# Kernel tuning notes

Measured on AMD Instinct MI355X. Metric: run time of the kernel, lower is better.

The kernel has to match this reference:

```python
import jax, jax.numpy as jnp
import numpy as np

TOP_K = 2


def setup_inputs() -> dict:
    key = jax.random.key(0)
    k1, k2, k3, k4, k5 = jax.random.split(key, 5)
    B, S, D, E, F = 2, 1024, 2048, 8, 768
    scale_in = 1.0 / np.sqrt(D)
    scale_ff = 1.0 / np.sqrt(F)
    return {
        "x": jax.random.normal(k1, (B, S, D), dtype=jnp.float32),
        "w_gate_router": jax.random.normal(k2, (E, D), dtype=jnp.float32) * scale_in,
        "w_gate_proj": jax.random.normal(k3, (E, F, D), dtype=jnp.float32) * scale_in,
        "w_up_proj": jax.random.normal(k4, (E, F, D), dtype=jnp.float32) * scale_in,
        "w_down_proj": jax.random.normal(k5, (E, D, F), dtype=jnp.float32) * scale_ff,
    }


def moe_forward(x, w_gate_router, w_gate_proj, w_up_proj, w_down_proj):
    E = w_gate_router.shape[0]
    # Router: scores [B,S,E], top-k selection, softmax over the k selected scores.
    scores = jnp.einsum("bsd,ed->bse", x, w_gate_router)
    topk_scores, topk_idx = jax.lax.top_k(scores, TOP_K)          # [B,S,K]
    topk_probs = jax.nn.softmax(topk_scores, axis=-1)             # [B,S,K]
    # Dense combine weights: zero for unselected experts (== scatter of topk_probs).
    weights = jnp.sum(topk_probs[..., None] * jax.nn.one_hot(topk_idx, E, dtype=x.dtype), axis=-2)  # [B,S,E]
    # Per-expert SwiGLU computed densely over all tokens (same math as
    # gather/dispatch-per-expert followed by scatter-add combine).
    gate = jnp.einsum("bsd,efd->bsef", x, w_gate_proj)            # [B,S,E,F]
    up = jnp.einsum("bsd,efd->bsef", x, w_up_proj)
    hidden = jax.nn.silu(gate) * up                                # [B,S,E,F]
    # Weighted combine: sum_e weights[b,s,e] * (hidden @ w_down[e].T)
    out = jnp.einsum("bsef,edf,bse->bsd", hidden, w_down_proj, weights)
    return out


def reference(x, w_gate_router, w_gate_proj, w_up_proj, w_down_proj):
    return moe_forward(x, w_gate_router, w_gate_proj, w_up_proj, w_down_proj)
```

## Files before the change

kernel.cpp:

```cpp
#include <hip/hip_runtime.h>

#define T_TOK 2048
#define DIM   2048
#define NEXP  8
#define FF    768
#define NGRP  16
#define BK    64

typedef unsigned short u16;
typedef unsigned int   u32;
typedef __bf16 bf16x8 __attribute__((ext_vector_type(8)));
typedef float  f32x4  __attribute__((ext_vector_type(4)));
typedef u16    u16x4  __attribute__((ext_vector_type(4)));
typedef u16    u16x8  __attribute__((ext_vector_type(8)));

#define AS1 __attribute__((address_space(1)))
#define AS3 __attribute__((address_space(3)))

__device__ __forceinline__ u16 f2bf(float f) {
    union { u32 i; float f; } v; v.f = f;
    u32 r = v.i + 0x7FFF + ((v.i >> 16) & 1);
    return (u16)(r >> 16);
}
__device__ __forceinline__ float bf2f(u16 u) {
    union { u32 i; float f; } v; v.i = ((u32)u) << 16; return v.f;
}

__device__ __forceinline__ void gload16(const u16* g, u16* l) {
    __builtin_amdgcn_global_load_lds((const AS1 u32*)g, (AS3 u32*)l, 16, 0, 0);
}

__global__ void cvt3_kernel(const float* __restrict__ s0, u16* __restrict__ d0,
                            const float* __restrict__ s1, u16* __restrict__ d1,
                            const float* __restrict__ s2, u16* __restrict__ d2, int n4) {
    const float* s; u16* d;
    switch (blockIdx.y) {
        case 0: s = s0; d = d0; break;
        case 1: s = s1; d = d1; break;
        default: s = s2; d = d2; break;
    }
    int i = blockIdx.x * blockDim.x + threadIdx.x;
    int st = gridDim.x * blockDim.x;
    for (; i < n4; i += st) {
        f32x4 v = ((const f32x4*)s)[i];
        u16x4 o;
#pragma unroll
        for (int j = 0; j < 4; j++) o[j] = f2bf(v[j]);
        ((u16x4*)d)[i] = o;
    }
}

__global__ void router_kernel(const float* __restrict__ x, const float* __restrict__ wr,
                              int* cnt, int* rt_e, float* rt_p, u16* __restrict__ xb) {
    int wave = threadIdx.x >> 6, lane = threadIdx.x & 63;
    int t = blockIdx.x * 4 + wave;
    float xv[32];
#pragma unroll
    for (int i = 0; i < 32; i++) xv[i] = x[(size_t)t * DIM + i * 64 + lane];
#pragma unroll
    for (int i = 0; i < 32; i++) xb[(size_t)t * DIM + i * 64 + lane] = f2bf(xv[i]);
    float s[NEXP];
#pragma unroll
    for (int e = 0; e < NEXP; e++) {
        float acc = 0.f;
#pragma unroll
        for (int i = 0; i < 32; i++) acc += xv[i] * wr[(size_t)e * DIM + i * 64 + lane];
        for (int off = 32; off; off >>= 1) acc += __shfl_xor(acc, off);
        s[e] = acc;
    }
    if (lane == 0) {
        int bi = 0; float bv = s[0];
        for (int e = 1; e < NEXP; e++) if (s[e] > bv) { bv = s[e]; bi = e; }
        float sv = -1e30f; int si = 0;
        for (int e = 0; e < NEXP; e++) { if (e == bi) continue; if (s[e] > sv) { sv = s[e]; si = e; } }
        float p0 = 1.f / (1.f + __expf(sv - bv));
        float p1 = 1.f - p0;
        rt_e[t * 2 + 0] = bi; rt_e[t * 2 + 1] = si;
        rt_p[t * 2 + 0] = p0; rt_p[t * 2 + 1] = p1;
        atomicAdd(&cnt[bi * 2 + 0], 1);
        atomicAdd(&cnt[si * 2 + 1], 1);
    }
}

__global__ void scan_kernel(const int* cnt, int* base, int* tile_g, int* tile_m0, int* ntiles) {
    int lane = threadIdx.x;
    int c = (lane < NGRP) ? cnt[lane] : 0;
    int nt_g = (c + 127) >> 7;
    int pre = 0, tpre = 0;
    for (int i = 0; i < NGRP; i++) {
        int ci = __shfl(c, i), ti = __shfl(nt_g, i);
        if (i < lane) { pre += ci; tpre += ti; }
    }
    if (lane < NGRP) {
        base[lane] = pre;
        for (int j = 0; j < nt_g; j++) { tile_g[tpre + j] = lane; tile_m0[tpre + j] = j * 128; }
        if (lane == NGRP - 1) *ntiles = tpre + nt_g;
    }
}

__global__ void assign_kernel(const int* rt_e, const float* rt_p, const int* base,
                              int* poscnt, int* rowtok, float* rowprob) {
    int t = blockIdx.x * blockDim.x + threadIdx.x;
    if (t >= T_TOK) return;
    for (int k = 0; k < 2; k++) {
        int g = rt_e[t * 2 + k] * 2 + k;
        int pos = atomicAdd(&poscnt[g], 1);
        int row = base[g] + pos;
        rowtok[row] = t;
        rowprob[row] = rt_p[t * 2 + k];
    }
}

__launch_bounds__(256)
__global__ void gateup_kernel(const u16* __restrict__ xb, const u16* __restrict__ wgb,
                              const u16* __restrict__ wub,
                              const int* cnt, const int* base, const int* tile_g,
                              const int* tile_m0, const int* ntiles,
                              const int* rowtok, const float* rowprob,
                              u16* __restrict__ hidden) {
    int tile = blockIdx.x;
    if (tile >= *ntiles) return;
    int g = tile_g[tile], m0 = tile_m0[tile];
    int e = g >> 1;
    int f0 = blockIdx.y * 32;
    int cg = cnt[g], bg_ = base[g];

    __shared__ u16 As[2][128 * BK];
    __shared__ u16 Bs[2][64 * BK];
    __shared__ int   tks[128];
    __shared__ float ps[128];

    int tid = threadIdx.x;
    if (tid < 128) {
        int valid = (m0 + tid) < cg;
        tks[tid] = valid ? rowtok[bg_ + m0 + tid] : 0;
        ps[tid]  = valid ? rowprob[bg_ + m0 + tid] : 0.f;
    }
    __syncthreads();

    int wave = tid >> 6, lane = tid & 63;
    int quad = lane >> 4, l16 = lane & 15;
    int wr = wave >> 1, wc = wave & 1;

    int r8  = lane >> 3;
    int csw = ((lane & 7) ^ r8) * 8;

    const u16* gA[4]; int lA[4];
#pragma unroll
    for (int gi = 0; gi < 4; gi++) {
        int row = wave * 32 + gi * 8 + r8;
        gA[gi] = xb + (size_t)tks[row] * DIM + csw;
        lA[gi] = (wave * 32 + gi * 8) * BK;
    }
    const u16* bsrc = (wave & 1) ? wub : wgb;
    const u16* gB[2]; int lB[2];
#pragma unroll
    for (int gi = 0; gi < 2; gi++) {
        int f = f0 + (wave >> 1) * 16 + gi * 8 + r8;
        gB[gi] = bsrc + ((size_t)e * FF + f) * DIM + csw;
        lB[gi] = (wave * 16 + gi * 8) * BK;
    }

    f32x4 acc[4][2] = {};

#pragma unroll
    for (int gi = 0; gi < 4; gi++) gload16(gA[gi], &As[0][0] + lA[gi]);
#pragma unroll
    for (int gi = 0; gi < 2; gi++) gload16(gB[gi], &Bs[0][0] + lB[gi]);
    __syncthreads();

    int sw0 = ((0 * 4 + quad) ^ (l16 & 7)) * 8;
    int sw1 = ((1 * 4 + quad) ^ (l16 & 7)) * 8;

#pragma unroll 2
    for (int kt = 0; kt < DIM / BK; kt++) {
        int cur = kt & 1;
        int kk = (kt + 1) * BK;
        if (kk < DIM) {
#pragma unroll
            for (int gi = 0; gi < 4; gi++) gload16(gA[gi] + kk, &As[cur ^ 1][0] + lA[gi]);
#pragma unroll
            for (int gi = 0; gi < 2; gi++) gload16(gB[gi] + kk, &Bs[cur ^ 1][0] + lB[gi]);
        }
#pragma unroll
        for (int ks = 0; ks < 2; ks++) {
            int sw = ks ? sw1 : sw0;
            bf16x8 a[4], b[2];
#pragma unroll
            for (int mi = 0; mi < 4; mi++)
                a[mi] = *(const bf16x8*)&As[cur][(wr * 64 + mi * 16 + l16) * BK + sw];
#pragma unroll
            for (int ni = 0; ni < 2; ni++)
                b[ni] = *(const bf16x8*)&Bs[cur][(wc * 32 + ni * 16 + l16) * BK + sw];
#pragma unroll
            for (int mi = 0; mi < 4; mi++)
#pragma unroll
                for (int ni = 0; ni < 2; ni++)
                    acc[mi][ni] = __builtin_amdgcn_mfma_f32_16x16x32_bf16(a[mi], b[ni], acc[mi][ni], 0, 0, 0);
        }
        __syncthreads();
    }

    int f = f0 + wc * 16 + l16;
#pragma unroll
    for (int mi = 0; mi < 4; mi++) {
#pragma unroll
        for (int r = 0; r < 4; r++) {
            int m = wr * 64 + mi * 16 + quad * 4 + r;
            if (m0 + m < cg) {
                float gv = acc[mi][0][r], uv = acc[mi][1][r];
                float h = (gv / (1.f + __expf(-gv))) * uv * ps[m];
                hidden[(size_t)(bg_ + m0 + m) * FF + f] = f2bf(h);
            }
        }
    }
}

__launch_bounds__(256)
__global__ void down_kernel(const u16* __restrict__ hid, const u16* __restrict__ wdb,
                            const int* cnt, const int* base, const int* tile_g,
                            const int* tile_m0, const int* ntiles, const int* rowtok,
                            u16* __restrict__ out0, u16* __restrict__ out1) {
    int tile = blockIdx.x;
    if (tile >= *ntiles) return;
    int g = tile_g[tile], m0 = tile_m0[tile];
    int e = g >> 1, slot = g & 1;
    int d0 = blockIdx.y * 64;
    int cg = cnt[g], bg_ = base[g];

    __shared__ u16 As[2][128 * BK];
    __shared__ u16 Bs[2][64 * BK];
    __shared__ int tks[128];

    int tid = threadIdx.x;
    if (tid < 128) tks[tid] = ((m0 + tid) < cg) ? rowtok[bg_ + m0 + tid] : 0;
    __syncthreads();

    int wave = tid >> 6, lane = tid & 63;
    int quad = lane >> 4, l16 = lane & 15;
    int wr = wave >> 1, wc = wave & 1;

    int r8  = lane >> 3;
    int csw = ((lane & 7) ^ r8) * 8;

    const u16* gA[4]; int lA[4];
#pragma unroll
    for (int gi = 0; gi < 4; gi++) {
        int row = wave * 32 + gi * 8 + r8;
        gA[gi] = hid + (size_t)(bg_ + m0 + row) * FF + csw;
        lA[gi] = (wave * 32 + gi * 8) * BK;
    }
    const u16* gB[2]; int lB[2];
#pragma unroll
    for (int gi = 0; gi < 2; gi++) {
        int n = wave * 16 + gi * 8 + r8;
        gB[gi] = wdb + ((size_t)e * DIM + d0 + n) * FF + csw;
        lB[gi] = (wave * 16 + gi * 8) * BK;
    }

    f32x4 acc[4][2] = {};

#pragma unroll
    for (int gi = 0; gi < 4; gi++) gload16(gA[gi], &As[0][0] + lA[gi]);
#pragma unroll
    for (int gi = 0; gi < 2; gi++) gload16(gB[gi], &Bs[0][0] + lB[gi]);
    __syncthreads();

    int sw0 = ((0 * 4 + quad) ^ (l16 & 7)) * 8;
    int sw1 = ((1 * 4 + quad) ^ (l16 & 7)) * 8;

#pragma unroll 2
    for (int kt = 0; kt < FF / BK; kt++) {
        int cur = kt & 1;
        int kk = (kt + 1) * BK;
        if (kk < FF) {
#pragma unroll
            for (int gi = 0; gi < 4; gi++) gload16(gA[gi] + kk, &As[cur ^ 1][0] + lA[gi]);
#pragma unroll
            for (int gi = 0; gi < 2; gi++) gload16(gB[gi] + kk, &Bs[cur ^ 1][0] + lB[gi]);
        }
#pragma unroll
        for (int ks = 0; ks < 2; ks++) {
            int sw = ks ? sw1 : sw0;
            bf16x8 a[4], b[2];
#pragma unroll
            for (int mi = 0; mi < 4; mi++)
                a[mi] = *(const bf16x8*)&As[cur][(wr * 64 + mi * 16 + l16) * BK + sw];
#pragma unroll
            for (int ni = 0; ni < 2; ni++)
                b[ni] = *(const bf16x8*)&Bs[cur][(wc * 32 + ni * 16 + l16) * BK + sw];
#pragma unroll
            for (int mi = 0; mi < 4; mi++)
#pragma unroll
                for (int ni = 0; ni < 2; ni++)
                    acc[mi][ni] = __builtin_amdgcn_mfma_f32_16x16x32_bf16(a[mi], b[ni], acc[mi][ni], 0, 0, 0);
        }
        __syncthreads();
    }

    u16* outp = slot ? out1 : out0;
#pragma unroll
    for (int mi = 0; mi < 4; mi++) {
#pragma unroll
        for (int ni = 0; ni < 2; ni++) {
            int d = d0 + wc * 32 + ni * 16 + l16;
#pragma unroll
            for (int r = 0; r < 4; r++) {
                int m = wr * 64 + mi * 16 + quad * 4 + r;
                if (m0 + m < cg) {
                    outp[(size_t)tks[m] * DIM + d] = f2bf(acc[mi][ni][r]);
                }
            }
        }
    }
}

__global__ void combine_kernel(const u16* __restrict__ o0, const u16* __restrict__ o1,
                               float* __restrict__ out) {
    int i = blockIdx.x * blockDim.x + threadIdx.x;
    u16x8 a = *(const u16x8*)(o0 + (size_t)i * 8);
    u16x8 b = *(const u16x8*)(o1 + (size_t)i * 8);
    f32x4 r0, r1;
#pragma unroll
    for (int j = 0; j < 4; j++) {
        r0[j] = bf2f(a[j]) + bf2f(b[j]);
        r1[j] = bf2f(a[4 + j]) + bf2f(b[4 + j]);
    }
    *(f32x4*)(out + (size_t)i * 8) = r0;
    *(f32x4*)(out + (size_t)i * 8 + 4) = r1;
}

extern "C" void kernel_launch(void* const* d_in, const int* in_sizes, int n_in,
                              void* d_out, int out_size, void* d_ws, size_t ws_size,
                              hipStream_t stream) {
    const float* x  = (const float*)d_in[0];
    const float* wr = (const float*)d_in[1];
    const float* wg = (const float*)d_in[2];
    const float* wu = (const float*)d_in[3];
    const float* wd = (const float*)d_in[4];
    float* out = (float*)d_out;

    char* W = (char*)d_ws;
    int*   cnt     = (int*)(W + 0);
    int*   poscnt  = (int*)(W + 64);
    int*   base    = (int*)(W + 128);
    int*   ntiles  = (int*)(W + 192);
    int*   tile_g  = (int*)(W + 256);
    int*   tile_m0 = (int*)(W + 512);
    int*   rt_e    = (int*)(W + 1024);
    float* rt_p    = (float*)(W + 20480);
    int*   rowtok  = (int*)(W + 40960);
    float* rowprob = (float*)(W + 61440);
    u16*   hidden  = (u16*)(W + 81920);
    u16*   xb      = (u16*)(W + ((size_t)8  << 20));
    u16*   wgb     = (u16*)(W + ((size_t)17 << 20));
    u16*   wub     = (u16*)(W + ((size_t)43 << 20));
    u16*   wdb     = (u16*)(W + ((size_t)69 << 20));
    u16*   out0    = (u16*)(W + ((size_t)17 << 20));
    u16*   out1    = (u16*)(W + ((size_t)26 << 20));

    hipMemsetAsync(W, 0, 256, stream);

    const int NW = NEXP * FF * DIM / 4;
    cvt3_kernel<<<dim3(1536, 3), 256, 0, stream>>>(wg, wgb, wu, wub, wd, wdb, NW);

    router_kernel<<<T_TOK / 4, 256, 0, stream>>>(x, wr, cnt, rt_e, rt_p, xb);
    scan_kernel<<<1, 64, 0, stream>>>(cnt, base, tile_g, tile_m0, ntiles);
    assign_kernel<<<8, 256, 0, stream>>>(rt_e, rt_p, base, poscnt, rowtok, rowprob);

    gateup_kernel<<<dim3(48, 24), 256, 0, stream>>>(xb, wgb, wub, cnt, base, tile_g, tile_m0,
                                                    ntiles, rowtok, rowprob, hidden);
    down_kernel<<<dim3(48, 32), 256, 0, stream>>>(hidden, wdb, cnt, base, tile_g, tile_m0,
                                                  ntiles, rowtok, out0, out1);
    combine_kernel<<<T_TOK * DIM / (256 * 8), 256, 0, stream>>>(out0, out1, out);
}
```

Baseline: 369.7 us.

## Fuse router with weight conversion, merge scan/assign, widen GEMM N tiles to 128

The router now runs as an extra grid row of the weight-conversion kernel, and the scan and assign steps share one kernel that uses shared-memory atomics. Together this removes two launches. The gate/up and down GEMM kernels double their N tile (64 gate+up columns, 128 output columns) with a 4x4 MFMA accumulator per wave. This raises reuse of the gathered A tile and halves the grid. The cost is more registers and LDS per block and fewer blocks, which may reduce occupancy and load balance.

Result: no change. 362.5 us (-1.9%).

```diff
diff --git a/kernel.cpp b/kernel.cpp
--- a/kernel.cpp
+++ b/kernel.cpp
@@ -30,14 +30,48 @@
     __builtin_amdgcn_global_load_lds((const AS1 u32*)g, (AS3 u32*)l, 16, 0, 0);
 }
 
-__global__ void cvt3_kernel(const float* __restrict__ s0, u16* __restrict__ d0,
-                            const float* __restrict__ s1, u16* __restrict__ d1,
-                            const float* __restrict__ s2, u16* __restrict__ d2, int n4) {
+__global__ void cvtrouter_kernel(const float* __restrict__ x, const float* __restrict__ wr,
+                                 int* cnt, int* rt_e, float* rt_p, u16* __restrict__ xb,
+                                 const float* __restrict__ wg, u16* __restrict__ wgb,
+                                 const float* __restrict__ wu, u16* __restrict__ wub,
+                                 const float* __restrict__ wd, u16* __restrict__ wdb, int n4) {
+    if (blockIdx.y == 0) {
+        if (blockIdx.x >= T_TOK / 4) return;
+        int wave = threadIdx.x >> 6, lane = threadIdx.x & 63;
+        int t = blockIdx.x * 4 + wave;
+        float xv[32];
+#pragma unroll
+        for (int i = 0; i < 32; i++) xv[i] = x[(size_t)t * DIM + i * 64 + lane];
+#pragma unroll
+        for (int i = 0; i < 32; i++) xb[(size_t)t * DIM + i * 64 + lane] = f2bf(xv[i]);
+        float s[NEXP];
+#pragma unroll
+        for (int e = 0; e < NEXP; e++) {
+            float acc = 0.f;
+#pragma unroll
+            for (int i = 0; i < 32; i++) acc += xv[i] * wr[(size_t)e * DIM + i * 64 + lane];
+            for (int off = 32; off; off >>= 1) acc += __shfl_xor(acc, off);
+            s[e] = acc;
+        }
+        if (lane == 0) {
+            int bi = 0; float bv = s[0];
+            for (int e = 1; e < NEXP; e++) if (s[e] > bv) { bv = s[e]; bi = e; }
+            float sv = -1e30f; int si = 0;
+            for (int e = 0; e < NEXP; e++) { if (e == bi) continue; if (s[e] > sv) { sv = s[e]; si = e; } }
+            float p0 = 1.f / (1.f + __expf(sv - bv));
+            float p1 = 1.f - p0;
+            rt_e[t * 2 + 0] = bi; rt_e[t * 2 + 1] = si;
+            rt_p[t * 2 + 0] = p0; rt_p[t * 2 + 1] = p1;
+            atomicAdd(&cnt[bi * 2 + 0], 1);
+            atomicAdd(&cnt[si * 2 + 1], 1);
+        }
+        return;
+    }
     const float* s; u16* d;
     switch (blockIdx.y) {
-        case 0: s = s0; d = d0; break;
-        case 1: s = s1; d = d1; break;
-        default: s = s2; d = d2; break;
+        case 1: s = wg; d = wgb; break;
+        case 2: s = wu; d = wub; break;
+        default: s = wd; d = wdb; break;
     }
     int i = blockIdx.x * blockDim.x + threadIdx.x;
     int st = gridDim.x * blockDim.x;
@@ -50,64 +84,38 @@
     }
 }
 
-__global__ void router_kernel(const float* __restrict__ x, const float* __restrict__ wr,
-                              int* cnt, int* rt_e, float* rt_p, u16* __restrict__ xb) {
-    int wave = threadIdx.x >> 6, lane = threadIdx.x & 63;
-    int t = blockIdx.x * 4 + wave;
-    float xv[32];
-#pragma unroll
-    for (int i = 0; i < 32; i++) xv[i] = x[(size_t)t * DIM + i * 64 + lane];
-#pragma unroll
-    for (int i = 0; i < 32; i++) xb[(size_t)t * DIM + i * 64 + lane] = f2bf(xv[i]);
-    float s[NEXP];
-#pragma unroll
-    for (int e = 0; e < NEXP; e++) {
-        float acc = 0.f;
-#pragma unroll
-        for (int i = 0; i < 32; i++) acc += xv[i] * wr[(size_t)e * DIM + i * 64 + lane];
-        for (int off = 32; off; off >>= 1) acc += __shfl_xor(acc, off);
-        s[e] = acc;
-    }
-    if (lane == 0) {
-        int bi = 0; float bv = s[0];
-        for (int e = 1; e < NEXP; e++) if (s[e] > bv) { bv = s[e]; bi = e; }
-        float sv = -1e30f; int si = 0;
-        for (int e = 0; e < NEXP; e++) { if (e == bi) continue; if (s[e] > sv) { sv = s[e]; si = e; } }
-        float p0 = 1.f / (1.f + __expf(sv - bv));
-        float p1 = 1.f - p0;
-        rt_e[t * 2 + 0] = bi; rt_e[t * 2 + 1] = si;
-        rt_p[t * 2 + 0] = p0; rt_p[t * 2 + 1] = p1;
-        atomicAdd(&cnt[bi * 2 + 0], 1);
-        atomicAdd(&cnt[si * 2 + 1], 1);
-    }
-}
-
-__global__ void scan_kernel(const int* cnt, int* base, int* tile_g, int* tile_m0, int* ntiles) {
-    int lane = threadIdx.x;
-    int c = (lane < NGRP) ? cnt[lane] : 0;
-    int nt_g = (c + 127) >> 7;
-    int pre = 0, tpre = 0;
-    for (int i = 0; i < NGRP; i++) {
-        int ci = __shfl(c, i), ti = __shfl(nt_g, i);
-        if (i < lane) { pre += ci; tpre += ti; }
-    }
-    if (lane < NGRP) {
-        base[lane] = pre;
-        for (int j = 0; j < nt_g; j++) { tile_g[tpre + j] = lane; tile_m0[tpre + j] = j * 128; }
-        if (lane == NGRP - 1) *ntiles = tpre + nt_g;
-    }
-}
-
-__global__ void assign_kernel(const int* rt_e, const float* rt_p, const int* base,
-                              int* poscnt, int* rowtok, float* rowprob) {
-    int t = blockIdx.x * blockDim.x + threadIdx.x;
-    if (t >= T_TOK) return;
-    for (int k = 0; k < 2; k++) {
-        int g = rt_e[t * 2 + k] * 2 + k;
-        int pos = atomicAdd(&poscnt[g], 1);
-        int row = base[g] + pos;
-        rowtok[row] = t;
-        rowprob[row] = rt_p[t * 2 + k];
+__global__ void scanassign_kernel(const int* cnt, const int* rt_e, const float* rt_p,
+                                  int* base_g, int* tile_g, int* tile_m0, int* ntiles,
+                                  int* rowtok, float* rowprob) {
+    __shared__ int s_base[NGRP];
+    __shared__ int s_pos[NGRP];
+    int tid = threadIdx.x;
+    if (tid < NGRP) s_pos[tid] = 0;
+    if (tid < 64) {
+        int lane = tid;
+        int c = (lane < NGRP) ? cnt[lane] : 0;
+        int nt_g = (c + 127) >> 7;
+        int pre = 0, tpre = 0;
+        for (int i = 0; i < NGRP; i++) {
+            int ci = __shfl(c, i), ti = __shfl(nt_g, i);
+            if (i < lane) { pre += ci; tpre += ti; }
+        }
+        if (lane < NGRP) {
+            s_base[lane] = pre; base_g[lane] = pre;
+            for (int j = 0; j < nt_g; j++) { tile_g[tpre + j] = lane; tile_m0[tpre + j] = j * 128; }
+            if (lane == NGRP - 1) *ntiles = tpre + nt_g;
+        }
+    }
+    __syncthreads();
+    for (int t = tid; t < T_TOK; t += 256) {
+#pragma unroll
+        for (int k = 0; k < 2; k++) {
+            int g = rt_e[t * 2 + k] * 2 + k;
+            int pos = atomicAdd(&s_pos[g], 1);
+            int row = s_base[g] + pos;
+            rowtok[row] = t;
+            rowprob[row] = rt_p[t * 2 + k];
+        }
     }
 }
 
@@ -122,11 +130,11 @@
     if (tile >= *ntiles) return;
     int g = tile_g[tile], m0 = tile_m0[tile];
     int e = g >> 1;
-    int f0 = blockIdx.y * 32;
+    int f0 = blockIdx.y * 64;
     int cg = cnt[g], bg_ = base[g];
 
     __shared__ u16 As[2][128 * BK];
-    __shared__ u16 Bs[2][64 * BK];
+    __shared__ u16 Bs[2][128 * BK];
     __shared__ int   tks[128];
     __shared__ float ps[128];
 
@@ -152,21 +160,21 @@
         gA[gi] = xb + (size_t)tks[row] * DIM + csw;
         lA[gi] = (wave * 32 + gi * 8) * BK;
     }
-    const u16* bsrc = (wave & 1) ? wub : wgb;
-    const u16* gB[2]; int lB[2];
-#pragma unroll
-    for (int gi = 0; gi < 2; gi++) {
-        int f = f0 + (wave >> 1) * 16 + gi * 8 + r8;
-        gB[gi] = bsrc + ((size_t)e * FF + f) * DIM + csw;
-        lB[gi] = (wave * 16 + gi * 8) * BK;
-    }
-
-    f32x4 acc[4][2] = {};
+    const u16* bsrc = (wave >> 1) ? wub : wgb;
+    int fo = (wave & 1) * 8 + r8;
+    const u16* gB[4]; int lB[4];
+#pragma unroll
+    for (int gi = 0; gi < 4; gi++) {
+        gB[gi] = bsrc + ((size_t)e * FF + f0 + gi * 16 + fo) * DIM + csw;
+        lB[gi] = (gi * 32 + wave * 8) * BK;
+    }
+
+    f32x4 acc[4][4] = {};
 
 #pragma unroll
     for (int gi = 0; gi < 4; gi++) gload16(gA[gi], &As[0][0] + lA[gi]);
 #pragma unroll
-    for (int gi = 0; gi < 2; gi++) gload16(gB[gi], &Bs[0][0] + lB[gi]);
+    for (int gi = 0; gi < 4; gi++) gload16(gB[gi], &Bs[0][0] + lB[gi]);
     __syncthreads();
 
     int sw0 = ((0 * 4 + quad) ^ (l16 & 7)) * 8;
@@ -180,37 +188,40 @@
 #pragma unroll
             for (int gi = 0; gi < 4; gi++) gload16(gA[gi] + kk, &As[cur ^ 1][0] + lA[gi]);
 #pragma unroll
-            for (int gi = 0; gi < 2; gi++) gload16(gB[gi] + kk, &Bs[cur ^ 1][0] + lB[gi]);
+            for (int gi = 0; gi < 4; gi++) gload16(gB[gi] + kk, &Bs[cur ^ 1][0] + lB[gi]);
         }
 #pragma unroll
         for (int ks = 0; ks < 2; ks++) {
             int sw = ks ? sw1 : sw0;
-            bf16x8 a[4], b[2];
+            bf16x8 a[4], b[4];
 #pragma unroll
             for (int mi = 0; mi < 4; mi++)
                 a[mi] = *(const bf16x8*)&As[cur][(wr * 64 + mi * 16 + l16) * BK + sw];
 #pragma unroll
-            for (int ni = 0; ni < 2; ni++)
-                b[ni] = *(const bf16x8*)&Bs[cur][(wc * 32 + ni * 16 + l16) * BK + sw];
+            for (int ni = 0; ni < 4; ni++)
+                b[ni] = *(const bf16x8*)&Bs[cur][(wc * 64 + ni * 16 + l16) * BK + sw];
 #pragma unroll
             for (int mi = 0; mi < 4; mi++)
 #pragma unroll
-                for (int ni = 0; ni < 2; ni++)
+                for (int ni = 0; ni < 4; ni++)
                     acc[mi][ni] = __builtin_amdgcn_mfma_f32_16x16x32_bf16(a[mi], b[ni], acc[mi][ni], 0, 0, 0);
         }
         __syncthreads();
     }
 
-    int f = f0 + wc * 16 + l16;
+    int fb = f0 + wc * 32 + l16;
 #pragma unroll
     for (int mi = 0; mi < 4; mi++) {
 #pragma unroll
         for (int r = 0; r < 4; r++) {
             int m = wr * 64 + mi * 16 + quad * 4 + r;
             if (m0 + m < cg) {
-                float gv = acc[mi][0][r], uv = acc[mi][1][r];
-                float h = (gv / (1.f + __expf(-gv))) * uv * ps[m];
-                hidden[(size_t)(bg_ + m0 + m) * FF + f] = f2bf(h);
+                float p = ps[m];
+                float g0 = acc[mi][0][r], u0 = acc[mi][1][r];
+                float g1 = acc[mi][2][r], u1 = acc[mi][3][r];
+                size_t rowo = (size_t)(bg_ + m0 + m) * FF;
+                hidden[rowo + fb]      = f2bf((g0 / (1.f + __expf(-g0))) * u0 * p);
+                hidden[rowo + fb + 16] = f2bf((g1 / (1.f + __expf(-g1))) * u1 * p);
             }
         }
     }
@@ -225,11 +236,11 @@
     if (tile >= *ntiles) return;
     int g = tile_g[tile], m0 = tile_m0[tile];
     int e = g >> 1, slot = g & 1;
-    int d0 = blockIdx.y * 64;
+    int d0 = blockIdx.y * 128;
     int cg = cnt[g], bg_ = base[g];
 
     __shared__ u16 As[2][128 * BK];
-    __shared__ u16 Bs[2][64 * BK];
+    __shared__ u16 Bs[2][128 * BK];
     __shared__ int tks[128];
 
     int tid = threadIdx.x;
@@ -250,20 +261,20 @@
         gA[gi] = hid + (size_t)(bg_ + m0 + row) * FF + csw;
         lA[gi] = (wave * 32 + gi * 8) * BK;
     }
-    const u16* gB[2]; int lB[2];
-#pragma unroll
-    for (int gi = 0; gi < 2; gi++) {
-        int n = wave * 16 + gi * 8 + r8;
+    const u16* gB[4]; int lB[4];
+#pragma unroll
+    for (int gi = 0; gi < 4; gi++) {
+        int n = gi * 32 + wave * 8 + r8;
         gB[gi] = wdb + ((size_t)e * DIM + d0 + n) * FF + csw;
-        lB[gi] = (wave * 16 + gi * 8) * BK;
-    }
-
-    f32x4 acc[4][2] = {};
+        lB[gi] = (gi * 32 + wave * 8) * BK;
+    }
+
+    f32x4 acc[4][4] = {};
 
 #pragma unroll
     for (int gi = 0; gi < 4; gi++) gload16(gA[gi], &As[0][0] + lA[gi]);
 #pragma unroll
-    for (int gi = 0; gi < 2; gi++) gload16(gB[gi], &Bs[0][0] + lB[gi]);
+    for (int gi = 0; gi < 4; gi++) gload16(gB[gi], &Bs[0][0] + lB[gi]);
     __syncthreads();
 
     int sw0 = ((0 * 4 + quad) ^ (l16 & 7)) * 8;
@@ -277,22 +288,22 @@
 #pragma unroll
             for (int gi = 0; gi < 4; gi++) gload16(gA[gi] + kk, &As[cur ^ 1][0] + lA[gi]);
 #pragma unroll
-            for (int gi = 0; gi < 2; gi++) gload16(gB[gi] + kk, &Bs[cur ^ 1][0] + lB[gi]);
+            for (int gi = 0; gi < 4; gi++) gload16(gB[gi] + kk, &Bs[cur ^ 1][0] + lB[gi]);
         }
 #pragma unroll
         for (int ks = 0; ks < 2; ks++) {
             int sw = ks ? sw1 : sw0;
-            bf16x8 a[4], b[2];
+            bf16x8 a[4], b[4];
 #pragma unroll
             for (int mi = 0; mi < 4; mi++)
                 a[mi] = *(const bf16x8*)&As[cur][(wr * 64 + mi * 16 + l16) * BK + sw];
 #pragma unroll
-            for (int ni = 0; ni < 2; ni++)
-                b[ni] = *(const bf16x8*)&Bs[cur][(wc * 32 + ni * 16 + l16) * BK + sw];
+            for (int ni = 0; ni < 4; ni++)
+                b[ni] = *(const bf16x8*)&Bs[cur][(wc * 64 + ni * 16 + l16) * BK + sw];
 #pragma unroll
             for (int mi = 0; mi < 4; mi++)
 #pragma unroll
-                for (int ni = 0; ni < 2; ni++)
+                for (int ni = 0; ni < 4; ni++)
                     acc[mi][ni] = __builtin_amdgcn_mfma_f32_16x16x32_bf16(a[mi], b[ni], acc[mi][ni], 0, 0, 0);
         }
         __syncthreads();
@@ -302,8 +313,8 @@
 #pragma unroll
     for (int mi = 0; mi < 4; mi++) {
 #pragma unroll
-        for (int ni = 0; ni < 2; ni++) {
-            int d = d0 + wc * 32 + ni * 16 + l16;
+        for (int ni = 0; ni < 4; ni++) {
+            int d = d0 + wc * 64 + ni * 16 + l16;
 #pragma unroll
             for (int r = 0; r < 4; r++) {
                 int m = wr * 64 + mi * 16 + quad * 4 + r;
@@ -342,7 +353,6 @@
 
     char* W = (char*)d_ws;
     int*   cnt     = (int*)(W + 0);
-    int*   poscnt  = (int*)(W + 64);
     int*   base    = (int*)(W + 128);
     int*   ntiles  = (int*)(W + 192);
     int*   tile_g  = (int*)(W + 256);
@@ -362,15 +372,14 @@
     hipMemsetAsync(W, 0, 256, stream);
 
     const int NW = NEXP * FF * DIM / 4;
-    cvt3_kernel<<<dim3(1536, 3), 256, 0, stream>>>(wg, wgb, wu, wub, wd, wdb, NW);
-
-    router_kernel<<<T_TOK / 4, 256, 0, stream>>>(x, wr, cnt, rt_e, rt_p, xb);
-    scan_kernel<<<1, 64, 0, stream>>>(cnt, base, tile_g, tile_m0, ntiles);
-    assign_kernel<<<8, 256, 0, stream>>>(rt_e, rt_p, base, poscnt, rowtok, rowprob);
-
-    gateup_kernel<<<dim3(48, 24), 256, 0, stream>>>(xb, wgb, wub, cnt, base, tile_g, tile_m0,
+    cvtrouter_kernel<<<dim3(1536, 4), 256, 0, stream>>>(x, wr, cnt, rt_e, rt_p, xb,
+                                                        wg, wgb, wu, wub, wd, wdb, NW);
+    scanassign_kernel<<<1, 256, 0, stream>>>(cnt, rt_e, rt_p, base, tile_g, tile_m0,
+                                             ntiles, rowtok, rowprob);
+
+    gateup_kernel<<<dim3(48, 12), 256, 0, stream>>>(xb, wgb, wub, cnt, base, tile_g, tile_m0,
                                                     ntiles, rowtok, rowprob, hidden);
-    down_kernel<<<dim3(48, 32), 256, 0, stream>>>(hidden, wdb, cnt, base, tile_g, tile_m0,
+    down_kernel<<<dim3(48, 16), 256, 0, stream>>>(hidden, wdb, cnt, base, tile_g, tile_m0,
                                                   ntiles, rowtok, out0, out1);
     combine_kernel<<<T_TOK * DIM / (256 * 8), 256, 0, stream>>>(out0, out1, out);
 }
```
